# Kernel tuning notes

Hardware: AMD Instinct MI355X
Metric: run time of the kernel (lower is better)

Reference implementation:

```python
import jax, jax.numpy as jnp
import numpy as np

N_HEAD = 32
D_MODEL = 4096
N_KV_GROUPS = 8
D_HEAD = D_MODEL // N_HEAD            # 128
H_PER_G = N_HEAD // N_KV_GROUPS       # 4
KV_DIM = N_KV_GROUPS * D_HEAD         # 1024
B, S = 2, 2048


def setup_inputs() -> dict:
    key = jax.random.key(0)
    ks = jax.random.split(key, 8)
    q = jax.random.normal(ks[0], (B, S, D_MODEL), dtype=jnp.float32)
    k = jax.random.normal(ks[1], (B, S, D_MODEL), dtype=jnp.float32)
    v = jax.random.normal(ks[2], (B, S, D_MODEL), dtype=jnp.float32)
    # causal mask (True = keep), broadcast over b, g, h as in the torch module
    mask = jnp.tril(jnp.ones((S, S), dtype=bool))
    # params: torch init is torch.rand (uniform [0,1)); scale down for numerics
    w_q = jax.random.uniform(ks[3], (D_MODEL, D_MODEL), dtype=jnp.float32) * 0.02
    w_k = jax.random.uniform(ks[4], (KV_DIM, D_MODEL), dtype=jnp.float32) * 0.02
    w_v = jax.random.uniform(ks[5], (KV_DIM, D_MODEL), dtype=jnp.float32) * 0.02
    w_out = jax.random.uniform(ks[6], (D_MODEL, D_MODEL), dtype=jnp.float32) * 0.02
    return {"q": q, "k": k, "v": v, "w_q": w_q, "w_k": w_k, "w_v": w_v,
            "w_out": w_out, "mask": mask}


def reference(q, k, v, w_q, w_k, w_v, w_out, mask):
    b, n, _ = q.shape
    s = k.shape[1]
    # F.linear(x, W) == x @ W.T
    query = q @ w_q.T                                  # [b, n, d_model]
    key = k @ w_k.T                                    # [b, s, kv_dim]
    value = v @ w_v.T                                  # [b, s, kv_dim]
    # b n (h d) -> b h n d -> b g h n d
    query = query.reshape(b, n, N_HEAD, D_HEAD).transpose(0, 2, 1, 3)
    query = query.reshape(b, N_KV_GROUPS, H_PER_G, n, D_HEAD)
    # b s (g d) -> b g s d
    key = key.reshape(b, s, N_KV_GROUPS, D_HEAD).transpose(0, 2, 1, 3)
    value = value.reshape(b, s, N_KV_GROUPS, D_HEAD).transpose(0, 2, 1, 3)
    scores = jnp.einsum('bghnd,bgsd->bghns', query, key) / (D_HEAD ** 0.5)
    scores = jnp.where(mask, scores, jnp.finfo(scores.dtype).min)
    attention = jax.nn.softmax(scores, axis=-1)        # [b, g, h, n, s]
    out = jnp.einsum('bghns,bgsd->bghnd', attention, value)
    # b g h n d -> b n (g h d)
    out = out.transpose(0, 3, 1, 2, 4).reshape(b, n, D_MODEL)
    return out @ w_out.T
```

## Files before the change

### kernel.cpp

```cpp
#include <hip/hip_runtime.h>

typedef unsigned short u16;
typedef unsigned int u32;
typedef __bf16 bf16x8 __attribute__((ext_vector_type(8)));
typedef float f32x4 __attribute__((ext_vector_type(4)));
typedef u16 u16x8 __attribute__((ext_vector_type(8)));
typedef u32 u32x2 __attribute__((ext_vector_type(2)));

#define SCL2E 0.12751744898229718f

__device__ __forceinline__ u16 f2bf(float f) {
  union { float f; u32 u; } x; x.f = f;
  u32 r = x.u + 0x7fffu + ((x.u >> 16) & 1u);
  return (u16)(r >> 16);
}

__device__ __forceinline__ u32 cvt_pk_bf16(float lo, float hi) {
  u32 r;
  asm("v_cvt_pk_bf16_f32 %0, %1, %2" : "=v"(r) : "v"(lo), "v"(hi));
  return r;
}

__device__ __forceinline__ void gld16(const void* g, void* l) {
  __builtin_amdgcn_global_load_lds(
      (const __attribute__((address_space(1))) u32*)g,
      (__attribute__((address_space(3))) u32*)l, 16, 0, 0);
}

#define SBAR() __builtin_amdgcn_s_barrier()
#define SCHEDB() __builtin_amdgcn_sched_barrier(0)
#define WAITVM(N) do { asm volatile("s_waitcnt vmcnt(" #N ")" ::: "memory"); \
                       __builtin_amdgcn_sched_barrier(0); } while (0)

#define STG(G, R0, DST, RIT, KT, K) do { \
    int rit_ = (RIT) + w*8 + lr; \
    int ch_ = lch ^ (rit_ & 7); \
    gld16((G) + ((R0) + rit_) * (long)(K) + (long)(KT)*64 + ch_*8, \
          (DST) + ((RIT) + w*8)*64); } while (0)

__device__ __forceinline__ void cvt_body(const float* __restrict__ in,
                                         u16* __restrict__ out, int n8) {
  int stride = gridDim.x * 256;
  for (int i = blockIdx.x * 256 + threadIdx.x; i < n8; i += stride) {
    float4 a = ((const float4*)in)[2*i];
    float4 b = ((const float4*)in)[2*i+1];
    u16x8 o;
    o[0]=f2bf(a.x); o[1]=f2bf(a.y); o[2]=f2bf(a.z); o[3]=f2bf(a.w);
    o[4]=f2bf(b.x); o[5]=f2bf(b.y); o[6]=f2bf(b.z); o[7]=f2bf(b.w);
    ((u16x8*)out)[i] = o;
  }
}

__global__ __launch_bounds__(256) void cvt3(
    const float* __restrict__ i0, const float* __restrict__ i1,
    const float* __restrict__ i2, u16* __restrict__ o0,
    u16* __restrict__ o1, u16* __restrict__ o2, int n8) {
  const float* in = blockIdx.y == 0 ? i0 : (blockIdx.y == 1 ? i1 : i2);
  u16* out = blockIdx.y == 0 ? o0 : (blockIdx.y == 1 ? o1 : o2);
  cvt_body(in, out, n8);
}

#define MFMA_(A, B, C) __builtin_amdgcn_mfma_f32_16x16x32_bf16(A, B, C, 0, 0, 0)

template<int OUTF32>
__device__ __forceinline__ void gemm256_body(
    const u16* __restrict__ Ag, const u16* __restrict__ Bg, void* __restrict__ Cp,
    const int K, const int ldc, const long m0, const long n0, const long cb,
    const float escale, u16* __restrict__ As, u16* __restrict__ Bs) {
  const int lane = threadIdx.x & 63, w = threadIdx.x >> 6;
  const int wm = w >> 2, wn = w & 3;
  const int c = lane & 15, grp = lane >> 4;
  const int lr = lane >> 3, lch = lane & 7;

  f32x4 acc[8][4] = {};
  const int NK = K >> 6;

  STG(Bg, n0, Bs, 0, 0, K);   STG(Bg, n0, Bs, 64, 0, K);
  STG(Bg, n0, Bs, 128, 0, K); STG(Bg, n0, Bs, 192, 0, K);
  STG(Ag, m0, As, 0, 0, K);   STG(Ag, m0, As, 64, 0, K);
  STG(Ag, m0, As, 128, 0, K); STG(Ag, m0, As, 192, 0, K);
  {
    u16* B1 = Bs + 16384;
    STG(Bg, n0, B1, 0, 1, K);   STG(Bg, n0, B1, 64, 1, K);
    STG(Bg, n0, B1, 128, 1, K); STG(Bg, n0, B1, 192, 1, K);
  }
  WAITVM(4);
  SBAR();

  for (int kt = 0; kt < NK; ++kt) {
    const u16* At = As + (kt & 1) * 16384;
    u16* An = As + ((kt & 1) ^ 1) * 16384;
    const u16* Bt = Bs + (kt % 3) * 16384;
    u16* Bn = Bs + ((kt + 2) % 3) * 16384;
    const bool am = (kt + 1 < NK), bm = (kt + 2 < NK);

    bf16x8 a0, a1, a2, a3, bfr[4];
#define LDAF(mi, ks) (*(const bf16x8*)(At + (wm*128 + (mi)*16 + c)*64 + ((((ks)*4 + grp)) ^ (c & 7))*8))
#define LDBF(ni, ks) (*(const bf16x8*)(Bt + (wn*64  + (ni)*16 + c)*64 + ((((ks)*4 + grp)) ^ (c & 7))*8))
#define MFMA16(MB) do { \
    __builtin_amdgcn_s_setprio(1); \
    _Pragma("unroll") \
    for (int ni = 0; ni < 4; ++ni) { \
      acc[(MB)+0][ni] = MFMA_(a0, bfr[ni], acc[(MB)+0][ni]); \
      acc[(MB)+1][ni] = MFMA_(a1, bfr[ni], acc[(MB)+1][ni]); \
      acc[(MB)+2][ni] = MFMA_(a2, bfr[ni], acc[(MB)+2][ni]); \
      acc[(MB)+3][ni] = MFMA_(a3, bfr[ni], acc[(MB)+3][ni]); \
    } \
    __builtin_amdgcn_s_setprio(0); } while (0)

    a0 = LDAF(0,0); a1 = LDAF(1,0); a2 = LDAF(2,0); a3 = LDAF(3,0);
    bfr[0] = LDBF(0,0); bfr[1] = LDBF(1,0); bfr[2] = LDBF(2,0); bfr[3] = LDBF(3,0);
    if (am) { STG(Ag, m0, An, 0, kt+1, K); STG(Ag, m0, An, 64, kt+1, K);
              STG(Ag, m0, An, 128, kt+1, K); STG(Ag, m0, An, 192, kt+1, K); }
    MFMA16(0);
    SCHEDB();
    a0 = LDAF(4,0); a1 = LDAF(5,0); a2 = LDAF(6,0); a3 = LDAF(7,0);
    if (bm) { STG(Bg, n0, Bn, 0, kt+2, K); STG(Bg, n0, Bn, 64, kt+2, K); }
    MFMA16(4);
    SCHEDB();
    a0 = LDAF(0,1); a1 = LDAF(1,1); a2 = LDAF(2,1); a3 = LDAF(3,1);
    bfr[0] = LDBF(0,1); bfr[1] = LDBF(1,1); bfr[2] = LDBF(2,1); bfr[3] = LDBF(3,1);
    if (bm) { STG(Bg, n0, Bn, 128, kt+2, K); STG(Bg, n0, Bn, 192, kt+2, K); }
    MFMA16(0);
    SCHEDB();
    a0 = LDAF(4,1); a1 = LDAF(5,1); a2 = LDAF(6,1); a3 = LDAF(7,1);
    MFMA16(4);
    if (bm) { WAITVM(4); } else { WAITVM(0); }
    SBAR();
    SCHEDB();
#undef MFMA16
#undef LDAF
#undef LDBF
  }

  #pragma unroll
  for (int mi = 0; mi < 8; ++mi) {
    #pragma unroll
    for (int rr = 0; rr < 4; ++rr) {
      long row = m0 + wm*128 + mi*16 + grp*4 + rr;
      #pragma unroll
      for (int ni = 0; ni < 4; ++ni) {
        long col = cb + wn*64 + ni*16 + c;
        if (OUTF32) ((float*)Cp)[row*ldc + col] = acc[mi][ni][rr];
        else        ((u16*)Cp)[row*ldc + col]  = f2bf(acc[mi][ni][rr] * escale);
      }
    }
  }
}

__device__ __forceinline__ void gemm128_body(
    const u16* __restrict__ Ag, const u16* __restrict__ Bg, u16* __restrict__ Cp,
    const int K, const int ldc, const long m0, const long n0, const long cb,
    u16* __restrict__ As, u16* __restrict__ Bs) {
  const int lane = threadIdx.x & 63, w = threadIdx.x >> 6;
  const int wm = w >> 2, wn = w & 3;
  const int c = lane & 15, grp = lane >> 4;
  const int lr = lane >> 3, lch = lane & 7;

  f32x4 acc[4][4] = {};
  const int NK = K >> 6;

  STG(Bg, n0, Bs, 0, 0, K);   STG(Bg, n0, Bs, 64, 0, K);
  STG(Bg, n0, Bs, 128, 0, K); STG(Bg, n0, Bs, 192, 0, K);
  STG(Ag, m0, As, 0, 0, K);   STG(Ag, m0, As, 64, 0, K);
  {
    u16* B1 = Bs + 16384; u16* A1 = As + 8192;
    STG(Bg, n0, B1, 0, 1, K);   STG(Bg, n0, B1, 64, 1, K);
    STG(Bg, n0, B1, 128, 1, K); STG(Bg, n0, B1, 192, 1, K);
    STG(Ag, m0, A1, 0, 1, K);   STG(Ag, m0, A1, 64, 1, K);
  }
  WAITVM(6);
  SBAR();

  for (int kt = 0; kt < NK; ++kt) {
    const u16* At = As + (kt % 3) * 8192;
    const u16* Bt = Bs + (kt % 3) * 16384;
    u16* An = As + ((kt + 2) % 3) * 8192;
    u16* Bn = Bs + ((kt + 2) % 3) * 16384;
    const bool bm = (kt + 2 < NK);

    bf16x8 a0, a1, a2, a3, bfr[4];
#define LDAF(mi, ks) (*(const bf16x8*)(At + (wm*64 + (mi)*16 + c)*64 + ((((ks)*4 + grp)) ^ (c & 7))*8))
#define LDBF(ni, ks) (*(const bf16x8*)(Bt + (wn*64 + (ni)*16 + c)*64 + ((((ks)*4 + grp)) ^ (c & 7))*8))
#define MFMA16K() do { \
    __builtin_amdgcn_s_setprio(1); \
    _Pragma("unroll") \
    for (int ni = 0; ni < 4; ++ni) { \
      acc[0][ni] = MFMA_(a0, bfr[ni], acc[0][ni]); \
      acc[1][ni] = MFMA_(a1, bfr[ni], acc[1][ni]); \
      acc[2][ni] = MFMA_(a2, bfr[ni], acc[2][ni]); \
      acc[3][ni] = MFMA_(a3, bfr[ni], acc[3][ni]); \
    } \
    __builtin_amdgcn_s_setprio(0); } while (0)

    a0 = LDAF(0,0); a1 = LDAF(1,0); a2 = LDAF(2,0); a3 = LDAF(3,0);
    bfr[0] = LDBF(0,0); bfr[1] = LDBF(1,0); bfr[2] = LDBF(2,0); bfr[3] = LDBF(3,0);
    if (bm) { STG(Bg, n0, Bn, 0, kt+2, K); STG(Bg, n0, Bn, 64, kt+2, K); }
    MFMA16K();
    SCHEDB();
    a0 = LDAF(0,1); a1 = LDAF(1,1); a2 = LDAF(2,1); a3 = LDAF(3,1);
    bfr[0] = LDBF(0,1); bfr[1] = LDBF(1,1); bfr[2] = LDBF(2,1); bfr[3] = LDBF(3,1);
    if (bm) { STG(Bg, n0, Bn, 128, kt+2, K); STG(Bg, n0, Bn, 192, kt+2, K);
              STG(Ag, m0, An, 0, kt+2, K); STG(Ag, m0, An, 64, kt+2, K); }
    MFMA16K();
    if (bm) { WAITVM(6); } else { WAITVM(0); }
    SBAR();
    SCHEDB();
#undef MFMA16K
#undef LDAF
#undef LDBF
  }

  #pragma unroll
  for (int mi = 0; mi < 4; ++mi) {
    #pragma unroll
    for (int rr = 0; rr < 4; ++rr) {
      long row = m0 + wm*64 + mi*16 + grp*4 + rr;
      #pragma unroll
      for (int ni = 0; ni < 4; ++ni) {
        long col = cb + wn*64 + ni*16 + c;
        Cp[row*ldc + col] = f2bf(acc[mi][ni][rr]);
      }
    }
  }
}

__global__ __launch_bounds__(512, 2) void proj_gemm(
    const u16* __restrict__ qb, const u16* __restrict__ kb,
    const u16* __restrict__ vb, const u16* __restrict__ wqb,
    const u16* __restrict__ wkv, u16* __restrict__ Qp, u16* __restrict__ KVp) {
  __shared__ __attribute__((aligned(16))) u16 SMEM[81920];
  int wg = ((int)blockIdx.x & 7) * 32 + ((int)blockIdx.x >> 3);
  gemm256_body<0>(qb, wqb, Qp, 4096, 4096,
                  (long)(wg >> 4) * 256, (long)(wg & 15) * 256, (long)(wg & 15) * 256,
                  SCL2E, SMEM, SMEM + 32768);
  {
    int mt = wg >> 3, nt = wg & 7;
    const u16* A_ = (nt < 4) ? kb : vb;
    const u16* B_ = wkv + ((nt < 4) ? 0 : 4194304);
    long n0 = (long)(nt & 3) * 256;
    long cb = (nt < 4) ? n0 : n0 + 1024;
    gemm128_body(A_, B_, KVp, 4096, 2048, (long)mt * 128, n0, cb,
                 SMEM, SMEM + 24576);
  }
}

__global__ __launch_bounds__(512, 2) void gemm_out(
    const u16* __restrict__ A, const u16* __restrict__ Bw, float* __restrict__ C) {
  __shared__ __attribute__((aligned(16))) u16 SMEM[81920];
  int wg = ((int)blockIdx.x & 7) * 32 + ((int)blockIdx.x >> 3);
  long m0 = (long)(wg >> 4) * 256, n0 = (long)(wg & 15) * 256;
  gemm256_body<1>(A, Bw, C, 4096, 4096, m0, n0, n0, 1.f, SMEM, SMEM + 32768);
}

__global__ __launch_bounds__(256) void transpose_v(
    const u16* __restrict__ KVp, u16* __restrict__ Vt) {
  const int s0 = blockIdx.x * 64, n0 = blockIdx.y * 64, b = blockIdx.z;
  const int tid = threadIdx.x;
  __shared__ __attribute__((aligned(16))) u16 t[64*80];
  #pragma unroll
  for (int p = 0; p < 2; ++p) {
    int sl = p*32 + (tid >> 3), nl = (tid & 7) * 8;
    *(u16x8*)(t + sl*80 + nl) =
        *(const u16x8*)(KVp + (long)(b*2048 + s0 + sl)*2048 + 1024 + n0 + nl);
  }
  __syncthreads();
  #pragma unroll
  for (int p = 0; p < 2; ++p) {
    int nl = p*32 + (tid >> 3), sc = (tid & 7) * 8;
    u16x8 o;
    #pragma unroll
    for (int j = 0; j < 8; ++j) o[j] = t[(sc + j)*80 + nl];
    *(u16x8*)(Vt + (long)(b*1024 + n0 + nl)*2048 + s0 + sc) = o;
  }
}

__global__ __launch_bounds__(512, 2) void attn_fwd(
    const u16* __restrict__ Qp, const u16* __restrict__ KVp,
    const u16* __restrict__ Vt, u16* __restrict__ AO) {
  const int head = blockIdx.y, b = blockIdx.z;
  const int g = head >> 2;
  const int tid = threadIdx.x, lane = tid & 63, w = tid >> 6;
  const int c = lane & 15, grp = lane >> 4;

  __shared__ __attribute__((aligned(16))) u16 Ks[2][64*128];
  __shared__ __attribute__((aligned(16))) u16 Vts[2][128*64];
  __shared__ __attribute__((aligned(16))) u16 Ps[8][32*64];
  u16* __restrict__ pw = &Ps[w][0];

  for (int half = 0; half < 2; ++half) {
    const int qt = half ? (7 - (int)blockIdx.x) : (int)blockIdx.x;
    const int q0 = qt * 256;
    const int qw = q0 + w * 32;

    bf16x8 qf[2][4];
    #pragma unroll
    for (int h = 0; h < 2; ++h) {
      const u16* qb = Qp + (long)(b*2048 + qw + h*16 + c)*4096 + head*128 + grp*8;
      #pragma unroll
      for (int t = 0; t < 4; ++t) qf[h][t] = *(const bf16x8*)(qb + t*32);
    }

    float m_run[2] = {-1e30f, -1e30f}, l_run[2] = {0.f, 0.f};
    f32x4 oacc[2][8] = {};

    const int ntiles = 4*qt + 4;

    auto STAGE = [&](int buf, int kt) {
      const int kv0 = kt * 64;
      #pragma unroll
      for (int p = 0; p < 2; ++p) {
        int idx = p*512 + w*64 + lane;
        int krow = idx >> 4, kc = idx & 15;
        int kcs = kc ^ (krow & 7);
        gld16(KVp + (long)(b*2048 + kv0 + krow)*2048 + g*128 + kcs*8,
              &Ks[buf][(p*512 + w*64)*8]);
        int d = idx >> 3, vc = idx & 7;
        int vcs = vc ^ (d & 7);
        gld16(Vt + (long)(b*1024 + g*128 + d)*2048 + kv0 + vcs*8,
              &Vts[buf][(p*512 + w*64)*8]);
      }
    };

    if (half) __syncthreads();
    STAGE(0, 0);
    int cur = 0;
    for (int kt = 0; kt < ntiles; ++kt) {
      const int kv0 = kt * 64;
      __syncthreads();
      if (kt + 1 < ntiles) STAGE(cur ^ 1, kt + 1);

      if (kv0 <= qw + 31) {
        const u16* __restrict__ Kc = &Ks[cur][0];
        const u16* __restrict__ Vc = &Vts[cur][0];

        f32x4 sacc[2][4] = {};
        __builtin_amdgcn_s_setprio(1);
        #pragma unroll
        for (int f = 0; f < 4; ++f) {
          const int row = f*16 + c;
          #pragma unroll
          for (int t = 0; t < 4; ++t) {
            bf16x8 kf = *(const bf16x8*)(Kc + row*128 + (((t*4 + grp) ^ (c & 7)) * 8));
            sacc[0][f] = __builtin_amdgcn_mfma_f32_16x16x32_bf16(kf, qf[0][t], sacc[0][f], 0, 0, 0);
            sacc[1][f] = __builtin_amdgcn_mfma_f32_16x16x32_bf16(kf, qf[1][t], sacc[1][f], 0, 0, 0);
          }
        }
        __builtin_amdgcn_s_setprio(0);

        #pragma unroll
        for (int h = 0; h < 2; ++h) {
          const int qg = qw + h*16 + c;
          float sv[16];
          if (kv0 + 63 > qw + h*16) {
            #pragma unroll
            for (int f = 0; f < 4; ++f)
              #pragma unroll
              for (int r = 0; r < 4; ++r) {
                float x = sacc[h][f][r];
                if (kv0 + f*16 + grp*4 + r > qg) x = -1e30f;
                sv[f*4 + r] = x;
              }
          } else {
            #pragma unroll
            for (int f = 0; f < 4; ++f)
              #pragma unroll
              for (int r = 0; r < 4; ++r) sv[f*4 + r] = sacc[h][f][r];
          }
          float tm[8];
          #pragma unroll
          for (int i = 0; i < 8; ++i) tm[i] = fmaxf(sv[i], sv[i+8]);
          #pragma unroll
          for (int i = 0; i < 4; ++i) tm[i] = fmaxf(tm[i], tm[i+4]);
          float tmax = fmaxf(fmaxf(tm[0], tm[2]), fmaxf(tm[1], tm[3]));
          tmax = fmaxf(tmax, __shfl_xor(tmax, 16));
          tmax = fmaxf(tmax, __shfl_xor(tmax, 32));

          float m_new = m_run[h];
          if (!__all(tmax <= m_run[h] + 8.f)) {
            m_new = fmaxf(m_run[h], tmax);
            float corr = exp2f(m_run[h] - m_new);
            l_run[h] *= corr;
            #pragma unroll
            for (int n = 0; n < 8; ++n) oacc[h][n] *= corr;
            m_run[h] = m_new;
          }

          float tsum = 0.f;
          u32 pk[8];
          #pragma unroll
          for (int i = 0; i < 8; ++i) {
            float p0 = exp2f(sv[2*i]   - m_new);
            float p1 = exp2f(sv[2*i+1] - m_new);
            tsum += p0 + p1;
            pk[i] = cvt_pk_bf16(p0, p1);
          }
          tsum += __shfl_xor(tsum, 16);
          tsum += __shfl_xor(tsum, 32);
          l_run[h] += tsum;

          #pragma unroll
          for (int f = 0; f < 4; ++f) {
            int col = (f*16 + grp*4) ^ ((c & 7) << 3);
            u32x2 pv; pv[0] = pk[2*f]; pv[1] = pk[2*f + 1];
            *(u32x2*)(pw + (h*16 + c)*64 + col) = pv;
          }
        }

        __builtin_amdgcn_s_setprio(1);
        #pragma unroll
        for (int u = 0; u < 2; ++u) {
          const int pcol = (u*32 + grp*8) ^ ((c & 7) << 3);
          bf16x8 pf0 = *(const bf16x8*)(pw + c*64 + pcol);
          bf16x8 pf1 = *(const bf16x8*)(pw + (16 + c)*64 + pcol);
          #pragma unroll
          for (int n = 0; n < 8; ++n) {
            bf16x8 vf = *(const bf16x8*)(Vc + (n*16 + c)*64 + (((u*4 + grp) ^ (c & 7)) * 8));
            oacc[0][n] = __builtin_amdgcn_mfma_f32_16x16x32_bf16(vf, pf0, oacc[0][n], 0, 0, 0);
            oacc[1][n] = __builtin_amdgcn_mfma_f32_16x16x32_bf16(vf, pf1, oacc[1][n], 0, 0, 0);
          }
        }
        __builtin_amdgcn_s_setprio(0);
      }
      cur ^= 1;
    }

    #pragma unroll
    for (int h = 0; h < 2; ++h) {
      const float inv = 1.0f / l_run[h];
      u16* ob = AO + (long)(b*2048 + qw + h*16 + c)*4096 + head*128 + grp*4;
      #pragma unroll
      for (int n = 0; n < 8; ++n) {
        u32x2 o;
        o[0] = cvt_pk_bf16(oacc[h][n][0]*inv, oacc[h][n][1]*inv);
        o[1] = cvt_pk_bf16(oacc[h][n][2]*inv, oacc[h][n][3]*inv);
        *(u32x2*)(ob + n*16) = o;
      }
    }
  }
}

extern "C" void kernel_launch(void* const* d_in, const int* in_sizes, int n_in,
                              void* d_out, int out_size, void* d_ws, size_t ws_size,
                              hipStream_t stream) {
  const float* q   = (const float*)d_in[0];
  const float* k   = (const float*)d_in[1];
  const float* v   = (const float*)d_in[2];
  const float* w_q = (const float*)d_in[3];
  const float* w_k = (const float*)d_in[4];
  const float* w_v = (const float*)d_in[5];
  const float* w_o = (const float*)d_in[6];

  u16* ws  = (u16*)d_ws;
  u16* qb  = ws;
  u16* kb  = qb  + 16777216;
  u16* vb  = kb  + 16777216;
  u16* wqb = vb  + 16777216;
  u16* wob = wqb + 16777216;
  u16* wkv = wob + 16777216;
  u16* Qp  = wkv + 8388608;
  u16* KVp = Qp  + 16777216;
  u16* Vtr = kb;
  u16* AO  = vb;
  (void)ws_size; (void)in_sizes; (void)n_in; (void)out_size;

  dim3 blk(256);
  cvt3<<<dim3(2048,3), blk, 0, stream>>>(q, k, v, qb, kb, vb, 2097152);
  cvt3<<<dim3(2048,2), blk, 0, stream>>>(w_q, w_o, w_o, wqb, wob, wob, 2097152);
  cvt3<<<dim3(512, 2), blk, 0, stream>>>(w_k, w_v, w_v, wkv, wkv + 4194304, wkv + 4194304, 524288);

  proj_gemm<<<256, dim3(512), 0, stream>>>(qb, kb, vb, wqb, wkv, Qp, KVp);
  transpose_v<<<dim3(32,16,2), blk, 0, stream>>>(KVp, Vtr);
  attn_fwd<<<dim3(4,32,2), dim3(512), 0, stream>>>(Qp, KVp, Vtr, AO);
  gemm_out<<<256, dim3(512), 0, stream>>>(AO, wob, (float*)d_out);
}
```

Measured before the change: 525.3 us.

## Fuse V transpose into projection GEMM epilogue and simplify GEMM double buffering

The V projection now writes its output directly in transposed layout from the GEMM epilogue, so the separate transpose_v kernel and its round trip through global memory go away. K is stored compactly with a 1024 stride, and attention addressing is updated to match. Both GEMM bodies also change from a three-deep B (and A) ring with partial waits to plain double buffering, issuing all loads for the next tile at the top and waiting for all of them at the end. That frees shared memory (81920 to 65536 elements) but gives less load/compute overlap. The transposed epilogue writes 4-element vectors along the sequence dimension, a strided global write pattern.

```diff
diff --git a/kernel.cpp b/kernel.cpp
--- a/kernel.cpp
+++ b/kernel.cpp
@@ -4,6 +4,7 @@
 typedef unsigned int u32;
 typedef __bf16 bf16x8 __attribute__((ext_vector_type(8)));
 typedef float f32x4 __attribute__((ext_vector_type(4)));
+typedef u16 u16x4 __attribute__((ext_vector_type(4)));
 typedef u16 u16x8 __attribute__((ext_vector_type(8)));
 typedef u32 u32x2 __attribute__((ext_vector_type(2)));
 
@@ -75,24 +76,28 @@
   f32x4 acc[8][4] = {};
   const int NK = K >> 6;
 
+  STG(Ag, m0, As, 0, 0, K);   STG(Ag, m0, As, 64, 0, K);
+  STG(Ag, m0, As, 128, 0, K); STG(Ag, m0, As, 192, 0, K);
   STG(Bg, n0, Bs, 0, 0, K);   STG(Bg, n0, Bs, 64, 0, K);
   STG(Bg, n0, Bs, 128, 0, K); STG(Bg, n0, Bs, 192, 0, K);
-  STG(Ag, m0, As, 0, 0, K);   STG(Ag, m0, As, 64, 0, K);
-  STG(Ag, m0, As, 128, 0, K); STG(Ag, m0, As, 192, 0, K);
-  {
-    u16* B1 = Bs + 16384;
-    STG(Bg, n0, B1, 0, 1, K);   STG(Bg, n0, B1, 64, 1, K);
-    STG(Bg, n0, B1, 128, 1, K); STG(Bg, n0, B1, 192, 1, K);
-  }
-  WAITVM(4);
+  WAITVM(0);
   SBAR();
+  SCHEDB();
 
   for (int kt = 0; kt < NK; ++kt) {
     const u16* At = As + (kt & 1) * 16384;
+    const u16* Bt = Bs + (kt & 1) * 16384;
     u16* An = As + ((kt & 1) ^ 1) * 16384;
-    const u16* Bt = Bs + (kt % 3) * 16384;
-    u16* Bn = Bs + ((kt + 2) % 3) * 16384;
-    const bool am = (kt + 1 < NK), bm = (kt + 2 < NK);
+    u16* Bn = Bs + ((kt & 1) ^ 1) * 16384;
+    const bool am = (kt + 1 < NK);
+
+    if (am) {
+      STG(Ag, m0, An, 0, kt+1, K);   STG(Ag, m0, An, 64, kt+1, K);
+      STG(Ag, m0, An, 128, kt+1, K); STG(Ag, m0, An, 192, kt+1, K);
+      STG(Bg, n0, Bn, 0, kt+1, K);   STG(Bg, n0, Bn, 64, kt+1, K);
+      STG(Bg, n0, Bn, 128, kt+1, K); STG(Bg, n0, Bn, 192, kt+1, K);
+    }
+    SCHEDB();
 
     bf16x8 a0, a1, a2, a3, bfr[4];
 #define LDAF(mi, ks) (*(const bf16x8*)(At + (wm*128 + (mi)*16 + c)*64 + ((((ks)*4 + grp)) ^ (c & 7))*8))
@@ -110,22 +115,16 @@
 
     a0 = LDAF(0,0); a1 = LDAF(1,0); a2 = LDAF(2,0); a3 = LDAF(3,0);
     bfr[0] = LDBF(0,0); bfr[1] = LDBF(1,0); bfr[2] = LDBF(2,0); bfr[3] = LDBF(3,0);
-    if (am) { STG(Ag, m0, An, 0, kt+1, K); STG(Ag, m0, An, 64, kt+1, K);
-              STG(Ag, m0, An, 128, kt+1, K); STG(Ag, m0, An, 192, kt+1, K); }
     MFMA16(0);
-    SCHEDB();
     a0 = LDAF(4,0); a1 = LDAF(5,0); a2 = LDAF(6,0); a3 = LDAF(7,0);
-    if (bm) { STG(Bg, n0, Bn, 0, kt+2, K); STG(Bg, n0, Bn, 64, kt+2, K); }
     MFMA16(4);
-    SCHEDB();
     a0 = LDAF(0,1); a1 = LDAF(1,1); a2 = LDAF(2,1); a3 = LDAF(3,1);
     bfr[0] = LDBF(0,1); bfr[1] = LDBF(1,1); bfr[2] = LDBF(2,1); bfr[3] = LDBF(3,1);
-    if (bm) { STG(Bg, n0, Bn, 128, kt+2, K); STG(Bg, n0, Bn, 192, kt+2, K); }
     MFMA16(0);
-    SCHEDB();
     a0 = LDAF(4,1); a1 = LDAF(5,1); a2 = LDAF(6,1); a3 = LDAF(7,1);
     MFMA16(4);
-    if (bm) { WAITVM(4); } else { WAITVM(0); }
+
+    WAITVM(0);
     SBAR();
     SCHEDB();
 #undef MFMA16
@@ -148,10 +147,11 @@
   }
 }
 
+template<int VOUT>
 __device__ __forceinline__ void gemm128_body(
     const u16* __restrict__ Ag, const u16* __restrict__ Bg, u16* __restrict__ Cp,
-    const int K, const int ldc, const long m0, const long n0, const long cb,
-    u16* __restrict__ As, u16* __restrict__ Bs) {
+    u16* __restrict__ Vt, const int K, const int ldc, const long m0, const long n0,
+    const long cb, u16* __restrict__ As, u16* __restrict__ Bs) {
   const int lane = threadIdx.x & 63, w = threadIdx.x >> 6;
   const int wm = w >> 2, wn = w & 3;
   const int c = lane & 15, grp = lane >> 4;
@@ -160,24 +160,26 @@
   f32x4 acc[4][4] = {};
   const int NK = K >> 6;
 
+  STG(Ag, m0, As, 0, 0, K);   STG(Ag, m0, As, 64, 0, K);
   STG(Bg, n0, Bs, 0, 0, K);   STG(Bg, n0, Bs, 64, 0, K);
   STG(Bg, n0, Bs, 128, 0, K); STG(Bg, n0, Bs, 192, 0, K);
-  STG(Ag, m0, As, 0, 0, K);   STG(Ag, m0, As, 64, 0, K);
-  {
-    u16* B1 = Bs + 16384; u16* A1 = As + 8192;
-    STG(Bg, n0, B1, 0, 1, K);   STG(Bg, n0, B1, 64, 1, K);
-    STG(Bg, n0, B1, 128, 1, K); STG(Bg, n0, B1, 192, 1, K);
-    STG(Ag, m0, A1, 0, 1, K);   STG(Ag, m0, A1, 64, 1, K);
-  }
-  WAITVM(6);
+  WAITVM(0);
   SBAR();
+  SCHEDB();
 
   for (int kt = 0; kt < NK; ++kt) {
-    const u16* At = As + (kt % 3) * 8192;
-    const u16* Bt = Bs + (kt % 3) * 16384;
-    u16* An = As + ((kt + 2) % 3) * 8192;
-    u16* Bn = Bs + ((kt + 2) % 3) * 16384;
-    const bool bm = (kt + 2 < NK);
+    const u16* At = As + (kt & 1) * 8192;
+    const u16* Bt = Bs + (kt & 1) * 16384;
+    u16* An = As + ((kt & 1) ^ 1) * 8192;
+    u16* Bn = Bs + ((kt & 1) ^ 1) * 16384;
+    const bool am = (kt + 1 < NK);
+
+    if (am) {
+      STG(Ag, m0, An, 0, kt+1, K);   STG(Ag, m0, An, 64, kt+1, K);
+      STG(Bg, n0, Bn, 0, kt+1, K);   STG(Bg, n0, Bn, 64, kt+1, K);
+      STG(Bg, n0, Bn, 128, kt+1, K); STG(Bg, n0, Bn, 192, kt+1, K);
+    }
+    SCHEDB();
 
     bf16x8 a0, a1, a2, a3, bfr[4];
 #define LDAF(mi, ks) (*(const bf16x8*)(At + (wm*64 + (mi)*16 + c)*64 + ((((ks)*4 + grp)) ^ (c & 7))*8))
@@ -195,15 +197,12 @@
 
     a0 = LDAF(0,0); a1 = LDAF(1,0); a2 = LDAF(2,0); a3 = LDAF(3,0);
     bfr[0] = LDBF(0,0); bfr[1] = LDBF(1,0); bfr[2] = LDBF(2,0); bfr[3] = LDBF(3,0);
-    if (bm) { STG(Bg, n0, Bn, 0, kt+2, K); STG(Bg, n0, Bn, 64, kt+2, K); }
     MFMA16K();
-    SCHEDB();
     a0 = LDAF(0,1); a1 = LDAF(1,1); a2 = LDAF(2,1); a3 = LDAF(3,1);
     bfr[0] = LDBF(0,1); bfr[1] = LDBF(1,1); bfr[2] = LDBF(2,1); bfr[3] = LDBF(3,1);
-    if (bm) { STG(Bg, n0, Bn, 128, kt+2, K); STG(Bg, n0, Bn, 192, kt+2, K);
-              STG(Ag, m0, An, 0, kt+2, K); STG(Ag, m0, An, 64, kt+2, K); }
     MFMA16K();
-    if (bm) { WAITVM(6); } else { WAITVM(0); }
+
+    WAITVM(0);
     SBAR();
     SCHEDB();
 #undef MFMA16K
@@ -211,15 +210,32 @@
 #undef LDBF
   }
 
-  #pragma unroll
-  for (int mi = 0; mi < 4; ++mi) {
+  if (VOUT == 0) {
     #pragma unroll
-    for (int rr = 0; rr < 4; ++rr) {
-      long row = m0 + wm*64 + mi*16 + grp*4 + rr;
+    for (int mi = 0; mi < 4; ++mi) {
+      #pragma unroll
+      for (int rr = 0; rr < 4; ++rr) {
+        long row = m0 + wm*64 + mi*16 + grp*4 + rr;
+        #pragma unroll
+        for (int ni = 0; ni < 4; ++ni) {
+          long col = cb + wn*64 + ni*16 + c;
+          Cp[row*ldc + col] = f2bf(acc[mi][ni][rr]);
+        }
+      }
+    }
+  } else {
+    #pragma unroll
+    for (int mi = 0; mi < 4; ++mi) {
+      long s_glob = m0 + wm*64 + mi*16 + grp*4;
+      long bb = s_glob >> 11;
+      long s_loc = s_glob & 2047;
       #pragma unroll
       for (int ni = 0; ni < 4; ++ni) {
-        long col = cb + wn*64 + ni*16 + c;
-        Cp[row*ldc + col] = f2bf(acc[mi][ni][rr]);
+        long feat = cb + wn*64 + ni*16 + c;
+        u16x4 o4;
+        #pragma unroll
+        for (int rr = 0; rr < 4; ++rr) o4[rr] = f2bf(acc[mi][ni][rr]);
+        *(u16x4*)(Vt + (bb*1024 + feat)*2048 + s_loc) = o4;
       }
     }
   }
@@ -228,51 +244,31 @@
 __global__ __launch_bounds__(512, 2) void proj_gemm(
     const u16* __restrict__ qb, const u16* __restrict__ kb,
     const u16* __restrict__ vb, const u16* __restrict__ wqb,
-    const u16* __restrict__ wkv, u16* __restrict__ Qp, u16* __restrict__ KVp) {
-  __shared__ __attribute__((aligned(16))) u16 SMEM[81920];
+    const u16* __restrict__ wkv, u16* __restrict__ Qp, u16* __restrict__ KVp,
+    u16* __restrict__ Vt) {
+  __shared__ __attribute__((aligned(16))) u16 SMEM[65536];
   int wg = ((int)blockIdx.x & 7) * 32 + ((int)blockIdx.x >> 3);
   gemm256_body<0>(qb, wqb, Qp, 4096, 4096,
                   (long)(wg >> 4) * 256, (long)(wg & 15) * 256, (long)(wg & 15) * 256,
                   SCL2E, SMEM, SMEM + 32768);
   {
     int mt = wg >> 3, nt = wg & 7;
-    const u16* A_ = (nt < 4) ? kb : vb;
-    const u16* B_ = wkv + ((nt < 4) ? 0 : 4194304);
     long n0 = (long)(nt & 3) * 256;
-    long cb = (nt < 4) ? n0 : n0 + 1024;
-    gemm128_body(A_, B_, KVp, 4096, 2048, (long)mt * 128, n0, cb,
-                 SMEM, SMEM + 24576);
+    if (nt < 4)
+      gemm128_body<0>(kb, wkv, KVp, nullptr, 4096, 1024, (long)mt * 128, n0, n0,
+                      SMEM, SMEM + 16384);
+    else
+      gemm128_body<1>(vb, wkv + 4194304, nullptr, Vt, 4096, 0, (long)mt * 128, n0, n0,
+                      SMEM, SMEM + 16384);
   }
 }
 
 __global__ __launch_bounds__(512, 2) void gemm_out(
     const u16* __restrict__ A, const u16* __restrict__ Bw, float* __restrict__ C) {
-  __shared__ __attribute__((aligned(16))) u16 SMEM[81920];
+  __shared__ __attribute__((aligned(16))) u16 SMEM[65536];
   int wg = ((int)blockIdx.x & 7) * 32 + ((int)blockIdx.x >> 3);
   long m0 = (long)(wg >> 4) * 256, n0 = (long)(wg & 15) * 256;
   gemm256_body<1>(A, Bw, C, 4096, 4096, m0, n0, n0, 1.f, SMEM, SMEM + 32768);
-}
-
-__global__ __launch_bounds__(256) void transpose_v(
-    const u16* __restrict__ KVp, u16* __restrict__ Vt) {
-  const int s0 = blockIdx.x * 64, n0 = blockIdx.y * 64, b = blockIdx.z;
-  const int tid = threadIdx.x;
-  __shared__ __attribute__((aligned(16))) u16 t[64*80];
-  #pragma unroll
-  for (int p = 0; p < 2; ++p) {
-    int sl = p*32 + (tid >> 3), nl = (tid & 7) * 8;
-    *(u16x8*)(t + sl*80 + nl) =
-        *(const u16x8*)(KVp + (long)(b*2048 + s0 + sl)*2048 + 1024 + n0 + nl);
-  }
-  __syncthreads();
-  #pragma unroll
-  for (int p = 0; p < 2; ++p) {
-    int nl = p*32 + (tid >> 3), sc = (tid & 7) * 8;
-    u16x8 o;
-    #pragma unroll
-    for (int j = 0; j < 8; ++j) o[j] = t[(sc + j)*80 + nl];
-    *(u16x8*)(Vt + (long)(b*1024 + n0 + nl)*2048 + s0 + sc) = o;
-  }
 }
 
 __global__ __launch_bounds__(512, 2) void attn_fwd(
@@ -313,7 +309,7 @@
         int idx = p*512 + w*64 + lane;
         int krow = idx >> 4, kc = idx & 15;
         int kcs = kc ^ (krow & 7);
-        gld16(KVp + (long)(b*2048 + kv0 + krow)*2048 + g*128 + kcs*8,
+        gld16(KVp + (long)(b*2048 + kv0 + krow)*1024 + g*128 + kcs*8,
               &Ks[buf][(p*512 + w*64)*8]);
         int d = idx >> 3, vc = idx & 7;
         int vcs = vc ^ (d & 7);
@@ -460,7 +456,7 @@
   u16* wkv = wob + 16777216;
   u16* Qp  = wkv + 8388608;
   u16* KVp = Qp  + 16777216;
-  u16* Vtr = kb;
+  u16* Vtp = KVp + 4194304;
   u16* AO  = vb;
   (void)ws_size; (void)in_sizes; (void)n_in; (void)out_size;
 
@@ -469,8 +465,7 @@
   cvt3<<<dim3(2048,2), blk, 0, stream>>>(w_q, w_o, w_o, wqb, wob, wob, 2097152);
   cvt3<<<dim3(512, 2), blk, 0, stream>>>(w_k, w_v, w_v, wkv, wkv + 4194304, wkv + 4194304, 524288);
 
-  proj_gemm<<<256, dim3(512), 0, stream>>>(qb, kb, vb, wqb, wkv, Qp, KVp);
-  transpose_v<<<dim3(32,16,2), blk, 0, stream>>>(KVp, Vtr);
-  attn_fwd<<<dim3(4,32,2), dim3(512), 0, stream>>>(Qp, KVp, Vtr, AO);
+  proj_gemm<<<256, dim3(512), 0, stream>>>(qb, kb, vb, wqb, wkv, Qp, KVp, Vtp);
+  attn_fwd<<<dim3(4,32,2), dim3(512), 0, stream>>>(Qp, KVp, Vtp, AO);
   gemm_out<<<256, dim3(512), 0, stream>>>(AO, wob, (float*)d_out);
 }
```

Result: slower. 537.8 us (+2.4%).
